# Kernel optimization log

Hardware: AMD Instinct MI355X
Metric: run time of the kernel (lower is better)

The kernel has to match this reference:

```python
import jax, jax.numpy as jnp
import numpy as np

N = 100000      # nodes
R = 3           # relations (num_relations)
E = 200000      # edges per relation
F_IN = 128      # in_channels
HID = 128       # hidden_channels
OUT = 64        # out_channels
H = 4           # attention heads


def setup_inputs() -> dict:
    key = jax.random.key(0)
    ks = jax.random.split(key, 16)
    s = lambda d: np.float32(1.0 / np.sqrt(d))
    x = jax.random.normal(ks[0], (N, F_IN), jnp.float32)
    edge_index = jax.random.randint(ks[1], (R, 2, E), 0, N)
    dh1, dh2 = HID // H, OUT // H
    # layer 1 params (in=128 -> hid=128)
    Wk1 = jax.random.normal(ks[2], (F_IN, HID), jnp.float32) * s(F_IN)
    Wq1 = jax.random.normal(ks[3], (F_IN, HID), jnp.float32) * s(F_IN)
    Wv1 = jax.random.normal(ks[4], (F_IN, HID), jnp.float32) * s(F_IN)
    A1 = jax.random.normal(ks[5], (R, H, dh1, dh1), jnp.float32) * s(dh1)  # per-relation attention transform
    M1 = jax.random.normal(ks[6], (R, H, dh1, dh1), jnp.float32) * s(dh1)  # per-relation message transform
    prior1 = jnp.ones((R, H), jnp.float32)  # relation priors mu
    Wo1 = jax.random.normal(ks[7], (HID, HID), jnp.float32) * s(HID)
    # layer 2 params (hid=128 -> out=64)
    Wk2 = jax.random.normal(ks[8], (HID, OUT), jnp.float32) * s(HID)
    Wq2 = jax.random.normal(ks[9], (HID, OUT), jnp.float32) * s(HID)
    Wv2 = jax.random.normal(ks[10], (HID, OUT), jnp.float32) * s(HID)
    A2 = jax.random.normal(ks[11], (R, H, dh2, dh2), jnp.float32) * s(dh2)
    M2 = jax.random.normal(ks[12], (R, H, dh2, dh2), jnp.float32) * s(dh2)
    prior2 = jnp.ones((R, H), jnp.float32)
    Wo2 = jax.random.normal(ks[13], (OUT, OUT), jnp.float32) * s(OUT)
    return dict(x=x, edge_index=edge_index,
                Wk1=Wk1, Wq1=Wq1, Wv1=Wv1, A1=A1, M1=M1, prior1=prior1, Wo1=Wo1,
                Wk2=Wk2, Wq2=Wq2, Wv2=Wv2, A2=A2, M2=M2, prior2=prior2, Wo2=Wo2)


def _hgt_conv(x, edge_index, Wk, Wq, Wv, A, M, prior, Wo):
    """Heterogeneous graph transformer conv: per-relation K/Q/V attention,
    dst-grouped segment softmax, scatter-add aggregation, output projection."""
    n = x.shape[0]
    d_out = Wk.shape[1]
    heads = A.shape[1]
    dh = d_out // heads
    k = (x @ Wk).reshape(n, heads, dh)
    q = (x @ Wq).reshape(n, heads, dh)
    v = (x @ Wv).reshape(n, heads, dh)
    src = edge_index[:, 0, :]  # [R,E]
    dst = edge_index[:, 1, :]  # [R,E]
    # per-relation transformed keys / messages on edges
    k_e = jnp.einsum('rehd,rhdf->rehf', k[src], A)          # [R,E,H,dh]
    msg = jnp.einsum('rehd,rhdf->rehf', v[src], M)          # [R,E,H,dh]
    score = jnp.einsum('rehf,rehf->reh', k_e, q[dst])
    score = score * prior[:, None, :] * np.float32(1.0 / np.sqrt(dh))
    # flatten all relations for a joint softmax over each destination node
    e_tot = src.size
    dst_f = dst.reshape(e_tot)
    score = score.reshape(e_tot, heads)
    msg = msg.reshape(e_tot, heads, dh)
    smax = jax.ops.segment_max(score, dst_f, num_segments=n)
    smax = jnp.where(jnp.isfinite(smax), smax, 0.0)         # nodes with no in-edges
    ex = jnp.exp(score - smax[dst_f])
    denom = jax.ops.segment_sum(ex, dst_f, num_segments=n)
    alpha = ex / (denom[dst_f] + 1e-9)                      # [E_tot,H]
    aggr = jax.ops.segment_sum(msg * alpha[..., None], dst_f, num_segments=n)
    return aggr.reshape(n, d_out) @ Wo


def reference(x, edge_index, Wk1, Wq1, Wv1, A1, M1, prior1, Wo1,
              Wk2, Wq2, Wv2, A2, M2, prior2, Wo2):
    h = _hgt_conv(x, edge_index, Wk1, Wq1, Wv1, A1, M1, prior1, Wo1)
    h = jax.nn.relu(h)
    return _hgt_conv(h, edge_index, Wk2, Wq2, Wv2, A2, M2, prior2, Wo2)
```

## Files before the change

### kernel.cpp

```cpp
#include <hip/hip_runtime.h>

#define NN 100000
#define RR 3
#define EE 200000
#define HH 4
#define ETOT (RR * EE)
#define NB ((NN + 255) / 256)

typedef __attribute__((ext_vector_type(8))) short bf16x8;
typedef __attribute__((ext_vector_type(4))) float f32x4;

__device__ __forceinline__ int clampi(int v, int lo, int hi) {
  return v < lo ? lo : (v > hi ? hi : v);
}

__device__ __forceinline__ void split2(float v, ushort& h, ushort& l) {
  uint u = __float_as_uint(v);
  uint hb = (u + 0x7FFFu + ((u >> 16) & 1u)) >> 16;
  float fh = __uint_as_float(hb << 16);
  float r = v - fh;
  uint ur = __float_as_uint(r);
  uint lb = (ur + 0x7FFFu + ((ur >> 16) & 1u)) >> 16;
  h = (ushort)hb; l = (ushort)lb;
}

__device__ __forceinline__ ushort f2bf(float v) {
  uint u = __float_as_uint(v);
  return (ushort)((u + 0x7FFFu + ((u >> 16) & 1u)) >> 16);
}

__global__ __launch_bounds__(256) void to_bf16(
    const float* __restrict__ A, ushort* __restrict__ Ah, int total8)
{
  int idx = blockIdx.x * 256 + threadIdx.x;
  if (idx >= total8) return;
  const float4* ap = (const float4*)(A + (size_t)idx * 8);
  float4 a0 = ap[0], a1 = ap[1];
  const float v[8] = {a0.x, a0.y, a0.z, a0.w, a1.x, a1.y, a1.z, a1.w};
  ushort h[8];
  #pragma unroll
  for (int i = 0; i < 8; ++i) h[i] = f2bf(v[i]);
  *(uint4*)(Ah + (size_t)idx * 8) = *(const uint4*)h;
}

template<int KT>
__global__ __launch_bounds__(256) void gemm_bf1(
    const ushort* __restrict__ Ah, const ushort* __restrict__ Bth,
    int M, int NTOT,
    ushort* __restrict__ kb, int nk, ushort* __restrict__ vb,
    ushort* __restrict__ qb, int nq, int reluq)
{
  constexpr int K = KT * 32;
  constexpr int LDB = KT * 16 + 4;
  __shared__ uint Bs[2][64 * LDB];
  const int tid = threadIdx.x;
  const int m0 = blockIdx.x * 128;
  const int lane = tid & 63, wv = tid >> 6;
  const int rbase = m0 + wv * 32 + (lane & 15);
  const int kof = (lane >> 4) * 8;

  bf16x8 a[2][KT];
  #pragma unroll
  for (int m = 0; m < 2; ++m) {
    const int row = rbase + m * 16;
    #pragma unroll
    for (int kt = 0; kt < KT; ++kt) {
      uint4 u = make_uint4(0, 0, 0, 0);
      if (row < M) u = *(const uint4*)(Ah + (size_t)row * K + kt * 32 + kof);
      a[m][kt] = *reinterpret_cast<bf16x8*>(&u);
    }
  }

  auto stage = [&](int cb, int b) {
    const int c = tid >> 2, kq = tid & 3;
    if (kq * 32 < K) {
      const uint4* s = (const uint4*)(Bth + (size_t)(cb + c) * K + kq * 32);
      uint4* d = (uint4*)&Bs[b][c * LDB + kq * 16];
      #pragma unroll
      for (int q = 0; q < 4; ++q) d[q] = s[q];
    }
  };
  stage(0, 0);
  __syncthreads();
  int buf = 0;

  for (int cb = 0; cb < NTOT; cb += 64) {
    if (cb + 64 < NTOT) stage(cb + 64, buf ^ 1);

    f32x4 acc[2][4];
    #pragma unroll
    for (int m = 0; m < 2; ++m)
      #pragma unroll
      for (int n = 0; n < 4; ++n) acc[m][n] = (f32x4){0.f, 0.f, 0.f, 0.f};

    #pragma unroll
    for (int kt = 0; kt < KT; ++kt) {
      #pragma unroll
      for (int n = 0; n < 4; ++n) {
        const int boff = (n * 16 + (lane & 15)) * LDB + kt * 16 + (lane >> 4) * 4;
        uint4 u = *(const uint4*)&Bs[buf][boff];
        bf16x8 b8 = *reinterpret_cast<bf16x8*>(&u);
        acc[0][n] = __builtin_amdgcn_mfma_f32_16x16x32_bf16(a[0][kt], b8, acc[0][n], 0, 0, 0);
        acc[1][n] = __builtin_amdgcn_mfma_f32_16x16x32_bf16(a[1][kt], b8, acc[1][n], 0, 0, 0);
      }
    }

    ushort* ob; int stride, cbase, relu = 0;
    if (cb < nk)            { ob = kb; stride = nk; cbase = cb; }
    else if (cb < 2 * nk)   { ob = vb; stride = nk; cbase = cb - nk; }
    else                    { ob = qb; stride = nq; cbase = cb - 2 * nk; relu = reluq; }
    #pragma unroll
    for (int m = 0; m < 2; ++m) {
      const int rw = m0 + wv * 32 + m * 16 + (lane >> 4) * 4;
      #pragma unroll
      for (int n = 0; n < 4; ++n) {
        const int col = cbase + n * 16 + (lane & 15);
        #pragma unroll
        for (int j = 0; j < 4; ++j) {
          if (rw + j < M) {
            float o = acc[m][n][j];
            if (relu) o = fmaxf(o, 0.f);
            ob[(size_t)(rw + j) * stride + col] = f2bf(o);
          }
        }
      }
    }
    __syncthreads();
    buf ^= 1;
  }
}

template<int KT>
__global__ __launch_bounds__(256) void gemm_sp3(
    const ushort* __restrict__ Ah, const ushort* __restrict__ Al,
    const ushort* __restrict__ Bth, const ushort* __restrict__ Btl,
    int M, int NTOT, float* __restrict__ of)
{
  constexpr int K = KT * 32;
  constexpr int LDB = KT * 16 + 4;
  __shared__ uint Bh[64 * LDB];
  __shared__ uint Bl[64 * LDB];
  const int tid = threadIdx.x;
  const int m0 = blockIdx.x * 128;
  const int lane = tid & 63, wv = tid >> 6;
  const int rbase = m0 + wv * 32 + (lane & 15);
  const int kof = (lane >> 4) * 8;

  bf16x8 ah[2][KT], al[2][KT];
  #pragma unroll
  for (int m = 0; m < 2; ++m) {
    const int row = rbase + m * 16;
    #pragma unroll
    for (int kt = 0; kt < KT; ++kt) {
      uint4 uh = make_uint4(0, 0, 0, 0), ul = make_uint4(0, 0, 0, 0);
      if (row < M) {
        uh = *(const uint4*)(Ah + (size_t)row * K + kt * 32 + kof);
        ul = *(const uint4*)(Al + (size_t)row * K + kt * 32 + kof);
      }
      ah[m][kt] = *reinterpret_cast<bf16x8*>(&uh);
      al[m][kt] = *reinterpret_cast<bf16x8*>(&ul);
    }
  }

  for (int cb = 0; cb < NTOT; cb += 64) {
    {
      const int c = tid >> 2, kq = tid & 3;
      if (kq * 32 < K) {
        const uint4* sh = (const uint4*)(Bth + (size_t)(cb + c) * K + kq * 32);
        const uint4* sl = (const uint4*)(Btl + (size_t)(cb + c) * K + kq * 32);
        uint4* dh = (uint4*)&Bh[c * LDB + kq * 16];
        uint4* dl = (uint4*)&Bl[c * LDB + kq * 16];
        #pragma unroll
        for (int q = 0; q < 4; ++q) { dh[q] = sh[q]; dl[q] = sl[q]; }
      }
    }
    __syncthreads();

    f32x4 acc[2][4];
    #pragma unroll
    for (int m = 0; m < 2; ++m)
      #pragma unroll
      for (int n = 0; n < 4; ++n) acc[m][n] = (f32x4){0.f, 0.f, 0.f, 0.f};

    #pragma unroll
    for (int kt = 0; kt < KT; ++kt) {
      #pragma unroll
      for (int n = 0; n < 4; ++n) {
        const int boff = (n * 16 + (lane & 15)) * LDB + kt * 16 + (lane >> 4) * 4;
        uint4 uh = *(const uint4*)&Bh[boff];
        uint4 ul = *(const uint4*)&Bl[boff];
        bf16x8 bh = *reinterpret_cast<bf16x8*>(&uh);
        bf16x8 bl = *reinterpret_cast<bf16x8*>(&ul);
        #pragma unroll
        for (int m = 0; m < 2; ++m) {
          acc[m][n] = __builtin_amdgcn_mfma_f32_16x16x32_bf16(ah[m][kt], bh, acc[m][n], 0, 0, 0);
          acc[m][n] = __builtin_amdgcn_mfma_f32_16x16x32_bf16(ah[m][kt], bl, acc[m][n], 0, 0, 0);
          acc[m][n] = __builtin_amdgcn_mfma_f32_16x16x32_bf16(al[m][kt], bh, acc[m][n], 0, 0, 0);
        }
      }
    }

    #pragma unroll
    for (int m = 0; m < 2; ++m) {
      const int rw = m0 + wv * 32 + m * 16 + (lane >> 4) * 4;
      #pragma unroll
      for (int n = 0; n < 4; ++n) {
        const int col = cb + n * 16 + (lane & 15);
        #pragma unroll
        for (int j = 0; j < 4; ++j)
          if (rw + j < M) of[(size_t)(rw + j) * NTOT + col] = acc[m][n][j];
      }
    }
    __syncthreads();
  }
}

__global__ __launch_bounds__(256) void convt(
    const float* __restrict__ W, ushort* __restrict__ Th, ushort* __restrict__ Tl,
    int K, int N)
{
  int idx = blockIdx.x * 256 + threadIdx.x;
  if (idx >= K * N) return;
  int n = idx / K, k = idx % K;
  ushort h, l; split2(W[(size_t)k * N + n], h, l);
  Th[(size_t)n * K + k] = h;
  Tl[(size_t)n * K + k] = l;
}

__global__ __launch_bounds__(256) void build_wT(
    const float* __restrict__ W, const float* __restrict__ T,
    ushort* __restrict__ Oh, ushort* __restrict__ Ol, int F, int D, int dh,
    const float* __restrict__ prior, float scale)
{
  const int cols = RR * D;
  int idx = blockIdx.x * 256 + threadIdx.x;
  if (idx >= F * cols) return;
  int i = idx / cols, c = idx % cols;
  int r = c / D, gf = c % D;
  int h = gf / dh, f = gf % dh;
  const float* w = W + (size_t)i * D + h * dh;
  const float* t = T + ((size_t)(r * HH + h) * dh) * dh + f;
  float s = 0.f;
  for (int d = 0; d < dh; ++d) s = fmaf(w[d], t[(size_t)d * dh], s);
  if (prior) s *= prior[r * HH + h] * scale;
  ushort hh, ll; split2(s, hh, ll);
  Oh[(size_t)c * F + i] = hh;
  Ol[(size_t)c * F + i] = ll;
}

__global__ __launch_bounds__(256) void zero_i32(int* __restrict__ p, int n)
{
  int i = blockIdx.x * 256 + threadIdx.x;
  if (i < n) p[i] = 0;
}

__global__ __launch_bounds__(256) void csr_count(
    const int* __restrict__ EI, int* __restrict__ cnt)
{
  int idx = blockIdx.x * 256 + threadIdx.x;
  if (idx >= ETOT) return;
  int r = idx / EE, e = idx % EE;
  int dst = clampi(EI[(size_t)r * 2 * EE + EE + e], 0, NN - 1);
  atomicAdd(&cnt[dst], 1);
}

__global__ __launch_bounds__(256) void scan_intra(
    int* __restrict__ arr, int* __restrict__ blksum)
{
  __shared__ int s[256];
  const int t = threadIdx.x;
  const int i = blockIdx.x * 256 + t;
  int v = (i < NN) ? arr[i] : 0;
  s[t] = v;
  __syncthreads();
  #pragma unroll
  for (int off = 1; off < 256; off <<= 1) {
    int x = (t >= off) ? s[t - off] : 0;
    __syncthreads();
    s[t] += x;
    __syncthreads();
  }
  if (i < NN) arr[i] = s[t] - v;
  if (t == 255) blksum[blockIdx.x] = s[255];
}

__global__ __launch_bounds__(256) void scan_mid(
    const int* __restrict__ blksum, int* __restrict__ blkoff)
{
  __shared__ int s[256];
  __shared__ int carry;
  const int t = threadIdx.x;
  if (t == 0) carry = 0;
  __syncthreads();
  for (int base = 0; base < NB; base += 256) {
    const int i = base + t;
    int v = (i < NB) ? blksum[i] : 0;
    s[t] = v;
    __syncthreads();
    #pragma unroll
    for (int off = 1; off < 256; off <<= 1) {
      int x = (t >= off) ? s[t - off] : 0;
      __syncthreads();
      s[t] += x;
      __syncthreads();
    }
    if (i < NB) blkoff[i] = carry + s[t] - v;
    __syncthreads();
    if (t == 255) carry += s[255];
    __syncthreads();
  }
}

__global__ __launch_bounds__(256) void scan_add(
    int* __restrict__ arr, const int* __restrict__ blkoff,
    int* __restrict__ rowptr, int* __restrict__ cursor)
{
  int i = blockIdx.x * 256 + threadIdx.x;
  if (i < NN) {
    int v = arr[i] + blkoff[i >> 8];
    rowptr[i] = v;
    cursor[i] = v;
  }
  if (i == NN) rowptr[NN] = ETOT;
}

__global__ __launch_bounds__(256) void csr_scatter(
    const int* __restrict__ EI, int* __restrict__ cursor,
    int* __restrict__ srcrel)
{
  int idx = blockIdx.x * 256 + threadIdx.x;
  if (idx >= ETOT) return;
  int r = idx / EE, e = idx % EE;
  int src = clampi(EI[(size_t)r * 2 * EE + e], 0, NN - 1);
  int dst = clampi(EI[(size_t)r * 2 * EE + EE + e], 0, NN - 1);
  int pos = atomicAdd(&cursor[dst], 1);
  pos = clampi(pos, 0, ETOT - 1);
  srcrel[pos] = src | (r << 24);
}

template<int D, int DH>
__global__ __launch_bounds__(256) void node_fused(
    const ushort* __restrict__ kb, const ushort* __restrict__ vb,
    const ushort* __restrict__ qb,
    const int* __restrict__ rowptr, const int* __restrict__ srcrel,
    ushort* __restrict__ agh, ushort* __restrict__ agl)
{
  constexpr int LPS = D / 4;
  constexpr int ES  = 64 / LPS;
  constexpr int SUB = DH / 4;
  const int lane = threadIdx.x & 63;
  const int wv = threadIdx.x >> 6;
  const int n = blockIdx.x * 4 + wv;
  if (n >= NN) return;
  const int slot = lane / LPS;
  const int sl   = lane % LPS;
  const uint2 qu = *(const uint2*)&qb[(size_t)n * D + sl * 4];
  const float q0 = __uint_as_float(qu.x << 16);
  const float q1 = __uint_as_float(qu.x & 0xFFFF0000u);
  const float q2 = __uint_as_float(qu.y << 16);
  const float q3 = __uint_as_float(qu.y & 0xFFFF0000u);
  const int j0 = clampi(rowptr[n], 0, ETOT);
  const int j1 = clampi(rowptr[n + 1], j0, ETOT);
  float a0 = 0.f, a1 = 0.f, a2 = 0.f, a3 = 0.f, den = 0.f;

  for (int jb = j0; jb < j1; jb += ES) {
    const int j = jb + slot;
    const bool valid = j < j1;
    const int jj = clampi(valid ? j : j0, 0, ETOT - 1);
    const int w = srcrel[jj];
    const int si = clampi(w & 0xFFFFFF, 0, NN - 1);
    const int r  = clampi(w >> 24, 0, RR - 1);
    const size_t base = (size_t)si * (RR * D) + r * D + sl * 4;
    const uint2 ku = *(const uint2*)&kb[base];
    const uint2 vu = *(const uint2*)&vb[base];
    float s =        __uint_as_float(ku.x << 16)          * q0;
    s = fmaf(__uint_as_float(ku.x & 0xFFFF0000u), q1, s);
    s = fmaf(__uint_as_float(ku.y << 16),         q2, s);
    s = fmaf(__uint_as_float(ku.y & 0xFFFF0000u), q3, s);
    #pragma unroll
    for (int off = SUB / 2; off >= 1; off >>= 1) s += __shfl_xor(s, off, 64);
    const float ex = valid ? __expf(s) : 0.f;
    den += ex;
    a0 = fmaf(ex, __uint_as_float(vu.x << 16),          a0);
    a1 = fmaf(ex, __uint_as_float(vu.x & 0xFFFF0000u),  a1);
    a2 = fmaf(ex, __uint_as_float(vu.y << 16),          a2);
    a3 = fmaf(ex, __uint_as_float(vu.y & 0xFFFF0000u),  a3);
  }

  #pragma unroll
  for (int off = LPS; off < 64; off <<= 1) {
    den += __shfl_xor(den, off, 64);
    a0 += __shfl_xor(a0, off, 64);
    a1 += __shfl_xor(a1, off, 64);
    a2 += __shfl_xor(a2, off, 64);
    a3 += __shfl_xor(a3, off, 64);
  }

  if (slot == 0) {
    const float inv = 1.f / (den + 1e-9f);
    const float o0 = a0 * inv, o1 = a1 * inv, o2 = a2 * inv, o3 = a3 * inv;
    if (agl) {
      ushort h0, l0, h1, l1, h2, l2, h3, l3;
      split2(o0, h0, l0); split2(o1, h1, l1);
      split2(o2, h2, l2); split2(o3, h3, l3);
      uint2 ho = make_uint2((uint)h0 | ((uint)h1 << 16), (uint)h2 | ((uint)h3 << 16));
      uint2 lo = make_uint2((uint)l0 | ((uint)l1 << 16), (uint)l2 | ((uint)l3 << 16));
      *(uint2*)&agh[(size_t)n * D + sl * 4] = ho;
      *(uint2*)&agl[(size_t)n * D + sl * 4] = lo;
    } else {
      uint2 ho = make_uint2((uint)f2bf(o0) | ((uint)f2bf(o1) << 16),
                            (uint)f2bf(o2) | ((uint)f2bf(o3) << 16));
      *(uint2*)&agh[(size_t)n * D + sl * 4] = ho;
    }
  }
}

extern "C" void kernel_launch(void* const* d_in, const int* in_sizes, int n_in,
                              void* d_out, int out_size, void* d_ws, size_t ws_size,
                              hipStream_t stream)
{
  const float* x   = (const float*)d_in[0];
  const int*   EI  = (const int*)  d_in[1];
  const float* Wk1 = (const float*)d_in[2];
  const float* Wq1 = (const float*)d_in[3];
  const float* Wv1 = (const float*)d_in[4];
  const float* A1  = (const float*)d_in[5];
  const float* M1  = (const float*)d_in[6];
  const float* P1  = (const float*)d_in[7];
  const float* Wo1 = (const float*)d_in[8];
  const float* Wk2 = (const float*)d_in[9];
  const float* Wq2 = (const float*)d_in[10];
  const float* Wv2 = (const float*)d_in[11];
  const float* A2  = (const float*)d_in[12];
  const float* M2  = (const float*)d_in[13];
  const float* P2  = (const float*)d_in[14];
  const float* Wo2 = (const float*)d_in[15];
  float* out = (float*)d_out;

  float* ws = (float*)d_ws;
  const size_t nd = (size_t)NN * 128;
  ushort* xh   = (ushort*)ws;
  ushort* agh  = xh;
  ushort* qb2  = (ushort*)ws;
  ushort* ag2h = (ushort*)(ws + nd / 4);
  ushort* qb1  = (ushort*)(ws + nd / 2);
  ushort* ag2l = (ushort*)(ws + nd / 2);
  ushort* kb   = (ushort*)(ws + nd);
  ushort* vb   = (ushort*)(ws + 5 * nd / 2);
  ushort* Hbh  = (ushort*)(ws + 4 * nd);
  ushort* WBth = (ushort*)(ws + 5 * nd);
  ushort* WBtl = WBth + 896 * 128;
  int* ints   = (int*)(WBtl + 896 * 128);
  int* rowptr = ints;
  int* cursor = rowptr + NN + 1;
  int* blks   = cursor + NN;
  int* srcrel = blks + 2 * NB;

  const size_t need_bytes = (5 * nd + 114688) * 4 +
      ((size_t)(NN + 1) + NN + 2 * NB + ETOT) * 4;
  if (ws_size < need_bytes) return;

  dim3 blk(256);
  const int GB = (NN + 127) / 128;
  const int NFB = (NN + 3) / 4;

  to_bf16<<<dim3((NN * 128 / 8 + 255) / 256), blk, 0, stream>>>(x, xh, NN * 128 / 8);
  build_wT<<<dim3(192), blk, 0, stream>>>(Wk1, A1, WBth, WBtl, 128, 128, 32,
                                          P1, 0.17677669529663687f);
  build_wT<<<dim3(192), blk, 0, stream>>>(Wv1, M1, WBth + 384 * 128, WBtl + 384 * 128,
                                          128, 128, 32, (const float*)nullptr, 1.f);
  convt<<<dim3(64), blk, 0, stream>>>(Wq1, WBth + 768 * 128, WBtl + 768 * 128, 128, 128);

  gemm_bf1<4><<<dim3(GB), blk, 0, stream>>>(xh, WBth, NN, 896, kb, 384, vb, qb1, 128, 0);

  zero_i32<<<dim3(NB), blk, 0, stream>>>(cursor, NN);
  csr_count<<<dim3((ETOT + 255) / 256), blk, 0, stream>>>(EI, cursor);
  scan_intra<<<dim3(NB), blk, 0, stream>>>(cursor, blks);
  scan_mid<<<dim3(1), blk, 0, stream>>>(blks, blks + NB);
  scan_add<<<dim3(NB), blk, 0, stream>>>(cursor, blks + NB, rowptr, cursor);
  csr_scatter<<<dim3((ETOT + 255) / 256), blk, 0, stream>>>(EI, cursor, srcrel);

  node_fused<128, 32><<<dim3(NFB), blk, 0, stream>>>(
      kb, vb, qb1, rowptr, srcrel, agh, (ushort*)nullptr);
  convt<<<dim3(64), blk, 0, stream>>>(Wo1, WBth, WBtl, 128, 128);
  gemm_bf1<4><<<dim3(GB), blk, 0, stream>>>(agh, WBth, NN, 128,
                                            (ushort*)nullptr, 0, (ushort*)nullptr,
                                            Hbh, 128, 1);

  build_wT<<<dim3(96), blk, 0, stream>>>(Wk2, A2, WBth, WBtl, 128, 64, 16,
                                         P2, 0.25f);
  build_wT<<<dim3(96), blk, 0, stream>>>(Wv2, M2, WBth + 192 * 128, WBtl + 192 * 128,
                                         128, 64, 16, (const float*)nullptr, 1.f);
  convt<<<dim3(32), blk, 0, stream>>>(Wq2, WBth + 384 * 128, WBtl + 384 * 128, 128, 64);
  gemm_bf1<4><<<dim3(GB), blk, 0, stream>>>(Hbh, WBth, NN, 448, kb, 192, vb, qb2, 64, 0);

  node_fused<64, 16><<<dim3(NFB), blk, 0, stream>>>(
      kb, vb, qb2, rowptr, srcrel, ag2h, ag2l);
  convt<<<dim3(16), blk, 0, stream>>>(Wo2, WBth, WBtl, 64, 64);
  gemm_sp3<2><<<dim3(GB), blk, 0, stream>>>(ag2h, ag2l, WBth, WBtl, NN, 64, out);
}
```

Before: 363.6 us.

## Merge all prep kernels into one launch and unroll node aggregation by two

All weight preprocessing kernels (build_wT, convt), the x-to-bf16 conversion and the cursor zeroing now run as one block-partitioned prep_all launch. Each weight now gets its own region of a larger workspace buffer, which removes eight or so small launches and the serial gaps between them. The node_fused edge loop is also unrolled to handle two edges per slot per iteration, so more independent gather loads are in flight. The cost is a larger weight workspace and higher register pressure in node_fused.

```diff
diff --git a/kernel.cpp b/kernel.cpp
--- a/kernel.cpp
+++ b/kernel.cpp
@@ -29,10 +29,10 @@
   return (ushort)((u + 0x7FFFu + ((u >> 16) & 1u)) >> 16);
 }
 
-__global__ __launch_bounds__(256) void to_bf16(
-    const float* __restrict__ A, ushort* __restrict__ Ah, int total8)
-{
-  int idx = blockIdx.x * 256 + threadIdx.x;
+__device__ __forceinline__ void to_bf16_body(
+    const float* __restrict__ A, ushort* __restrict__ Ah, int blk, int total8)
+{
+  int idx = blk * 256 + threadIdx.x;
   if (idx >= total8) return;
   const float4* ap = (const float4*)(A + (size_t)idx * 8);
   float4 a0 = ap[0], a1 = ap[1];
@@ -42,6 +42,72 @@
   for (int i = 0; i < 8; ++i) h[i] = f2bf(v[i]);
   *(uint4*)(Ah + (size_t)idx * 8) = *(const uint4*)h;
 }
+
+__device__ __forceinline__ void build_wT_body(
+    const float* __restrict__ W, const float* __restrict__ T,
+    ushort* __restrict__ Oh, ushort* __restrict__ Ol, int F, int D, int dh,
+    const float* __restrict__ prior, float scale, int blk)
+{
+  const int cols = RR * D;
+  int idx = blk * 256 + threadIdx.x;
+  if (idx >= F * cols) return;
+  int i = idx / cols, c = idx % cols;
+  int r = c / D, gf = c % D;
+  int h = gf / dh, f = gf % dh;
+  const float* w = W + (size_t)i * D + h * dh;
+  const float* t = T + ((size_t)(r * HH + h) * dh) * dh + f;
+  float s = 0.f;
+  for (int d = 0; d < dh; ++d) s = fmaf(w[d], t[(size_t)d * dh], s);
+  if (prior) s *= prior[r * HH + h] * scale;
+  ushort hh, ll; split2(s, hh, ll);
+  Oh[(size_t)c * F + i] = hh;
+  Ol[(size_t)c * F + i] = ll;
+}
+
+__device__ __forceinline__ void convt_body(
+    const float* __restrict__ W, ushort* __restrict__ Th, ushort* __restrict__ Tl,
+    int K, int N, int blk)
+{
+  int idx = blk * 256 + threadIdx.x;
+  if (idx >= K * N) return;
+  int n = idx / K, k = idx % K;
+  ushort h, l; split2(W[(size_t)k * N + n], h, l);
+  Th[(size_t)n * K + k] = h;
+  Tl[(size_t)n * K + k] = l;
+}
+
+__global__ __launch_bounds__(256) void prep_all(
+    const float* __restrict__ x, ushort* __restrict__ xh,
+    const float* __restrict__ Wk1, const float* __restrict__ A1, const float* __restrict__ P1,
+    const float* __restrict__ Wv1, const float* __restrict__ M1,
+    const float* __restrict__ Wq1, const float* __restrict__ Wo1,
+    const float* __restrict__ Wk2, const float* __restrict__ A2, const float* __restrict__ P2,
+    const float* __restrict__ Wv2, const float* __restrict__ M2,
+    const float* __restrict__ Wq2, const float* __restrict__ Wo2,
+    ushort* __restrict__ WBth, ushort* __restrict__ WBtl, int* __restrict__ cursor)
+{
+  int b = blockIdx.x;
+  if (b < 6250) { to_bf16_body(x, xh, b, NN * 128 / 8); return; }
+  b -= 6250;
+  if (b < NB) { int i = b * 256 + threadIdx.x; if (i < NN) cursor[i] = 0; return; }
+  b -= NB;
+  if (b < 192) { build_wT_body(Wk1, A1, WBth, WBtl, 128, 128, 32, P1, 0.17677669529663687f, b); return; }
+  b -= 192;
+  if (b < 192) { build_wT_body(Wv1, M1, WBth + 384 * 128, WBtl + 384 * 128, 128, 128, 32, (const float*)0, 1.f, b); return; }
+  b -= 192;
+  if (b < 64) { convt_body(Wq1, WBth + 768 * 128, WBtl + 768 * 128, 128, 128, b); return; }
+  b -= 64;
+  if (b < 64) { convt_body(Wo1, WBth + 896 * 128, WBtl + 896 * 128, 128, 128, b); return; }
+  b -= 64;
+  if (b < 96) { build_wT_body(Wk2, A2, WBth + 1024 * 128, WBtl + 1024 * 128, 128, 64, 16, P2, 0.25f, b); return; }
+  b -= 96;
+  if (b < 96) { build_wT_body(Wv2, M2, WBth + 1216 * 128, WBtl + 1216 * 128, 128, 64, 16, (const float*)0, 1.f, b); return; }
+  b -= 96;
+  if (b < 32) { convt_body(Wq2, WBth + 1408 * 128, WBtl + 1408 * 128, 128, 64, b); return; }
+  b -= 32;
+  if (b < 16) { convt_body(Wo2, WBth + 1472 * 128, WBtl + 1472 * 128, 64, 64, b); return; }
+}
+#define PREP_BLOCKS (6250 + NB + 192 + 192 + 64 + 64 + 96 + 96 + 32 + 16)
 
 template<int KT>
 __global__ __launch_bounds__(256) void gemm_bf1(
@@ -213,45 +279,6 @@
     }
     __syncthreads();
   }
-}
-
-__global__ __launch_bounds__(256) void convt(
-    const float* __restrict__ W, ushort* __restrict__ Th, ushort* __restrict__ Tl,
-    int K, int N)
-{
-  int idx = blockIdx.x * 256 + threadIdx.x;
-  if (idx >= K * N) return;
-  int n = idx / K, k = idx % K;
-  ushort h, l; split2(W[(size_t)k * N + n], h, l);
-  Th[(size_t)n * K + k] = h;
-  Tl[(size_t)n * K + k] = l;
-}
-
-__global__ __launch_bounds__(256) void build_wT(
-    const float* __restrict__ W, const float* __restrict__ T,
-    ushort* __restrict__ Oh, ushort* __restrict__ Ol, int F, int D, int dh,
-    const float* __restrict__ prior, float scale)
-{
-  const int cols = RR * D;
-  int idx = blockIdx.x * 256 + threadIdx.x;
-  if (idx >= F * cols) return;
-  int i = idx / cols, c = idx % cols;
-  int r = c / D, gf = c % D;
-  int h = gf / dh, f = gf % dh;
-  const float* w = W + (size_t)i * D + h * dh;
-  const float* t = T + ((size_t)(r * HH + h) * dh) * dh + f;
-  float s = 0.f;
-  for (int d = 0; d < dh; ++d) s = fmaf(w[d], t[(size_t)d * dh], s);
-  if (prior) s *= prior[r * HH + h] * scale;
-  ushort hh, ll; split2(s, hh, ll);
-  Oh[(size_t)c * F + i] = hh;
-  Ol[(size_t)c * F + i] = ll;
-}
-
-__global__ __launch_bounds__(256) void zero_i32(int* __restrict__ p, int n)
-{
-  int i = blockIdx.x * 256 + threadIdx.x;
-  if (i < n) p[i] = 0;
 }
 
 __global__ __launch_bounds__(256) void csr_count(
@@ -363,28 +390,48 @@
   const int j1 = clampi(rowptr[n + 1], j0, ETOT);
   float a0 = 0.f, a1 = 0.f, a2 = 0.f, a3 = 0.f, den = 0.f;
 
-  for (int jb = j0; jb < j1; jb += ES) {
-    const int j = jb + slot;
-    const bool valid = j < j1;
-    const int jj = clampi(valid ? j : j0, 0, ETOT - 1);
-    const int w = srcrel[jj];
-    const int si = clampi(w & 0xFFFFFF, 0, NN - 1);
-    const int r  = clampi(w >> 24, 0, RR - 1);
-    const size_t base = (size_t)si * (RR * D) + r * D + sl * 4;
-    const uint2 ku = *(const uint2*)&kb[base];
-    const uint2 vu = *(const uint2*)&vb[base];
-    float s =        __uint_as_float(ku.x << 16)          * q0;
-    s = fmaf(__uint_as_float(ku.x & 0xFFFF0000u), q1, s);
-    s = fmaf(__uint_as_float(ku.y << 16),         q2, s);
-    s = fmaf(__uint_as_float(ku.y & 0xFFFF0000u), q3, s);
-    #pragma unroll
-    for (int off = SUB / 2; off >= 1; off >>= 1) s += __shfl_xor(s, off, 64);
-    const float ex = valid ? __expf(s) : 0.f;
-    den += ex;
-    a0 = fmaf(ex, __uint_as_float(vu.x << 16),          a0);
-    a1 = fmaf(ex, __uint_as_float(vu.x & 0xFFFF0000u),  a1);
-    a2 = fmaf(ex, __uint_as_float(vu.y << 16),          a2);
-    a3 = fmaf(ex, __uint_as_float(vu.y & 0xFFFF0000u),  a3);
+  for (int jb = j0; jb < j1; jb += 2 * ES) {
+    const int jA = jb + slot;
+    const int jB = jb + ES + slot;
+    const bool vA = jA < j1, vB = jB < j1;
+    const int jjA = clampi(vA ? jA : j0, 0, ETOT - 1);
+    const int jjB = clampi(vB ? jB : j0, 0, ETOT - 1);
+    const int wA = srcrel[jjA];
+    const int wB = srcrel[jjB];
+    const int sA = clampi(wA & 0xFFFFFF, 0, NN - 1);
+    const int rA = clampi(wA >> 24, 0, RR - 1);
+    const int sB = clampi(wB & 0xFFFFFF, 0, NN - 1);
+    const int rB = clampi(wB >> 24, 0, RR - 1);
+    const size_t bA = (size_t)sA * (RR * D) + rA * D + sl * 4;
+    const size_t bB = (size_t)sB * (RR * D) + rB * D + sl * 4;
+    const uint2 kuA = *(const uint2*)&kb[bA];
+    const uint2 vuA = *(const uint2*)&vb[bA];
+    const uint2 kuB = *(const uint2*)&kb[bB];
+    const uint2 vuB = *(const uint2*)&vb[bB];
+    float sa =        __uint_as_float(kuA.x << 16)         * q0;
+    sa = fmaf(__uint_as_float(kuA.x & 0xFFFF0000u), q1, sa);
+    sa = fmaf(__uint_as_float(kuA.y << 16),         q2, sa);
+    sa = fmaf(__uint_as_float(kuA.y & 0xFFFF0000u), q3, sa);
+    float sb =        __uint_as_float(kuB.x << 16)         * q0;
+    sb = fmaf(__uint_as_float(kuB.x & 0xFFFF0000u), q1, sb);
+    sb = fmaf(__uint_as_float(kuB.y << 16),         q2, sb);
+    sb = fmaf(__uint_as_float(kuB.y & 0xFFFF0000u), q3, sb);
+    #pragma unroll
+    for (int off = SUB / 2; off >= 1; off >>= 1) {
+      sa += __shfl_xor(sa, off, 64);
+      sb += __shfl_xor(sb, off, 64);
+    }
+    const float exA = vA ? __expf(sa) : 0.f;
+    const float exB = vB ? __expf(sb) : 0.f;
+    den += exA + exB;
+    a0 = fmaf(exA, __uint_as_float(vuA.x << 16),         a0);
+    a1 = fmaf(exA, __uint_as_float(vuA.x & 0xFFFF0000u), a1);
+    a2 = fmaf(exA, __uint_as_float(vuA.y << 16),         a2);
+    a3 = fmaf(exA, __uint_as_float(vuA.y & 0xFFFF0000u), a3);
+    a0 = fmaf(exB, __uint_as_float(vuB.x << 16),         a0);
+    a1 = fmaf(exB, __uint_as_float(vuB.x & 0xFFFF0000u), a1);
+    a2 = fmaf(exB, __uint_as_float(vuB.y << 16),         a2);
+    a3 = fmaf(exB, __uint_as_float(vuB.y & 0xFFFF0000u), a3);
   }
 
   #pragma unroll
@@ -449,14 +496,14 @@
   ushort* vb   = (ushort*)(ws + 5 * nd / 2);
   ushort* Hbh  = (ushort*)(ws + 4 * nd);
   ushort* WBth = (ushort*)(ws + 5 * nd);
-  ushort* WBtl = WBth + 896 * 128;
-  int* ints   = (int*)(WBtl + 896 * 128);
+  ushort* WBtl = WBth + 1536 * 128;
+  int* ints   = (int*)(WBtl + 1536 * 128);
   int* rowptr = ints;
   int* cursor = rowptr + NN + 1;
   int* blks   = cursor + NN;
   int* srcrel = blks + 2 * NB;
 
-  const size_t need_bytes = (5 * nd + 114688) * 4 +
+  const size_t need_bytes = (5 * nd + 2 * 98304) * 4 +
       ((size_t)(NN + 1) + NN + 2 * NB + ETOT) * 4;
   if (ws_size < need_bytes) return;
 
@@ -464,16 +511,12 @@
   const int GB = (NN + 127) / 128;
   const int NFB = (NN + 3) / 4;
 
-  to_bf16<<<dim3((NN * 128 / 8 + 255) / 256), blk, 0, stream>>>(x, xh, NN * 128 / 8);
-  build_wT<<<dim3(192), blk, 0, stream>>>(Wk1, A1, WBth, WBtl, 128, 128, 32,
-                                          P1, 0.17677669529663687f);
-  build_wT<<<dim3(192), blk, 0, stream>>>(Wv1, M1, WBth + 384 * 128, WBtl + 384 * 128,
-                                          128, 128, 32, (const float*)nullptr, 1.f);
-  convt<<<dim3(64), blk, 0, stream>>>(Wq1, WBth + 768 * 128, WBtl + 768 * 128, 128, 128);
+  prep_all<<<dim3(PREP_BLOCKS), blk, 0, stream>>>(
+      x, xh, Wk1, A1, P1, Wv1, M1, Wq1, Wo1,
+      Wk2, A2, P2, Wv2, M2, Wq2, Wo2, WBth, WBtl, cursor);
 
   gemm_bf1<4><<<dim3(GB), blk, 0, stream>>>(xh, WBth, NN, 896, kb, 384, vb, qb1, 128, 0);
 
-  zero_i32<<<dim3(NB), blk, 0, stream>>>(cursor, NN);
   csr_count<<<dim3((ETOT + 255) / 256), blk, 0, stream>>>(EI, cursor);
   scan_intra<<<dim3(NB), blk, 0, stream>>>(cursor, blks);
   scan_mid<<<dim3(1), blk, 0, stream>>>(blks, blks + NB);
@@ -482,20 +525,16 @@
 
   node_fused<128, 32><<<dim3(NFB), blk, 0, stream>>>(
       kb, vb, qb1, rowptr, srcrel, agh, (ushort*)nullptr);
-  convt<<<dim3(64), blk, 0, stream>>>(Wo1, WBth, WBtl, 128, 128);
-  gemm_bf1<4><<<dim3(GB), blk, 0, stream>>>(agh, WBth, NN, 128,
+  gemm_bf1<4><<<dim3(GB), blk, 0, stream>>>(agh, WBth + 896 * 128, NN, 128,
                                             (ushort*)nullptr, 0, (ushort*)nullptr,
                                             Hbh, 128, 1);
 
-  build_wT<<<dim3(96), blk, 0, stream>>>(Wk2, A2, WBth, WBtl, 128, 64, 16,
-                                         P2, 0.25f);
-  build_wT<<<dim3(96), blk, 0, stream>>>(Wv2, M2, WBth + 192 * 128, WBtl + 192 * 128,
-                                         128, 64, 16, (const float*)nullptr, 1.f);
-  convt<<<dim3(32), blk, 0, stream>>>(Wq2, WBth + 384 * 128, WBtl + 384 * 128, 128, 64);
-  gemm_bf1<4><<<dim3(GB), blk, 0, stream>>>(Hbh, WBth, NN, 448, kb, 192, vb, qb2, 64, 0);
+  gemm_bf1<4><<<dim3(GB), blk, 0, stream>>>(Hbh, WBth + 1024 * 128, NN, 448,
+                                            kb, 192, vb, qb2, 64, 0);
 
   node_fused<64, 16><<<dim3(NFB), blk, 0, stream>>>(
       kb, vb, qb2, rowptr, srcrel, ag2h, ag2l);
-  convt<<<dim3(16), blk, 0, stream>>>(Wo2, WBth, WBtl, 64, 64);
-  gemm_sp3<2><<<dim3(GB), blk, 0, stream>>>(ag2h, ag2l, WBth, WBtl, NN, 64, out);
-}
+  gemm_sp3<2><<<dim3(GB), blk, 0, stream>>>(ag2h, ag2l,
+                                            WBth + 1472 * 128, WBtl + 1472 * 128,
+                                            NN, 64, out);
+}
```

After: 303.6 us. 1.2x faster.
